# Performance work log

Measured on AMD Instinct MI355X. Metric: run time of the kernel, lower is better.

## Reference

```python
import jax, jax.numpy as jnp
import numpy as np

T, B, N, N2 = 2048, 32, 1024, 512

def setup_inputs() -> dict:
    key = jax.random.key(0)
    ks = jax.random.split(key, 7)
    s_n = 1.0 / np.sqrt(N)
    s_n2 = 1.0 / np.sqrt(N2)
    return {
        "hyp": jax.random.normal(ks[0], (T, B, N), dtype=jnp.float32),
        "W_w": jax.random.uniform(ks[1], (N2, N), jnp.float32, -s_n, s_n),
        "W_b": jax.random.uniform(ks[2], (N2,), jnp.float32, -s_n, s_n),
        "Wm_w": jax.random.uniform(ks[3], (N2, N), jnp.float32, -s_n, s_n),
        "Wm_b": jax.random.uniform(ks[4], (N2,), jnp.float32, -s_n, s_n),
        "Wh_w": jax.random.uniform(ks[5], (1, N2), jnp.float32, -s_n2, s_n2),
        "Wh_b": jax.random.uniform(ks[6], (1,), jnp.float32, -s_n2, s_n2),
        "dan_hidden_size": N,
        "attention_hidden_size": N2,
    }

def reference(hyp, W_w, W_b, Wm_w, Wm_b, Wh_w, Wh_b, dan_hidden_size, attention_hidden_size):
    # attention_type == 'attention' branch
    m = jnp.mean(hyp, axis=0)                      # [B, N] mean over time
    x = jnp.transpose(hyp, (1, 0, 2))              # [B, T, N]
    hq = jnp.tanh(jnp.einsum('btn,kn->btk', x, W_w) + W_b)        # [B, T, N2]
    hm = jnp.tanh(m @ Wm_w.T + Wm_b)[:, None, :]   # [B, 1, N2]
    h = hq * hm                                    # [B, T, N2]
    score = jnp.einsum('btk,ok->bto', h, Wh_w) + Wh_b  # [B, T, 1]
    a = jax.nn.softmax(score, axis=1)              # softmax over T
    c = jnp.sum(a * x, axis=1)                     # [B, N]
    return c
```

## Files before the change

### kernel.cpp

```cpp
#include <hip/hip_runtime.h>
#include <hip/hip_bf16.h>

#define TDIM 2048
#define BDIM 32
#define NDIM 1024
#define N2DIM 512
#define BN (BDIM * NDIM)
#define LDSP 72
#define NPART 64

typedef float f32x4 __attribute__((ext_vector_type(4)));
typedef __bf16 bf16x8 __attribute__((ext_vector_type(8)));

__device__ __forceinline__ float bf2f(unsigned int u) {
    union { unsigned int i; float f; } c;
    c.i = (u & 0xffffu) << 16;
    return c.f;
}

__device__ __forceinline__ unsigned short f2bf(float f) {
    union { float f; unsigned int i; } c;
    c.f = f;
    unsigned int i = c.i;
    unsigned int r = (i >> 16) & 1u;
    i += 0x7fffu + r;
    return (unsigned short)(i >> 16);
}

__device__ __forceinline__ int detect_f32(const void* wb) {
    const unsigned short* p = (const unsigned short*)wb;
    int cnt = 0;
    #pragma unroll
    for (int i = 0; i < 64; ++i) cnt += ((p[i] & 0x7fffu) <= 0x3D00u) ? 1 : 0;
    return cnt != 64;
}

__device__ __forceinline__ float ldf(const void* p, size_t i, int isf32) {
    if (isf32) return ((const float*)p)[i];
    return bf2f(((const unsigned short*)p)[i]);
}

__device__ __forceinline__ float tanh_fast(float x) {
    float e = __expf(2.0f * x);
    return 1.0f - 2.0f / (e + 1.0f);
}

__device__ __forceinline__ void unpack8(uint4 u, float* f) {
    f[0] = bf2f(u.x); f[1] = bf2f(u.x >> 16);
    f[2] = bf2f(u.y); f[3] = bf2f(u.y >> 16);
    f[4] = bf2f(u.z); f[5] = bf2f(u.z >> 16);
    f[6] = bf2f(u.w); f[7] = bf2f(u.w >> 16);
}

__device__ __forceinline__ void async16(const void* g, void* l) {
    __builtin_amdgcn_global_load_lds(
        (const __attribute__((address_space(1))) void*)g,
        (__attribute__((address_space(3))) void*)l, 16, 0, 0);
}


__global__ __launch_bounds__(256) void k_mean_cvt(const void* __restrict__ hyp,
                                                  const void* __restrict__ wb,
                                                  unsigned short* __restrict__ hyp16,
                                                  float* __restrict__ part) {
    const int isf32 = detect_f32(wb);
    const int col4 = (blockIdx.x * 256 + threadIdx.x) * 4;
    const int tc   = blockIdx.y;
    float a0 = 0.f, a1 = 0.f, a2 = 0.f, a3 = 0.f;
    if (isf32) {
        const float* h = (const float*)hyp + (size_t)(tc * 32) * BN + col4;
        unsigned short* o = hyp16 + (size_t)(tc * 32) * BN + col4;
        #pragma unroll 8
        for (int tt = 0; tt < 32; ++tt) {
            float4 v = *(const float4*)(h + (size_t)tt * BN);
            a0 += v.x; a1 += v.y; a2 += v.z; a3 += v.w;
            ushort4 u = { f2bf(v.x), f2bf(v.y), f2bf(v.z), f2bf(v.w) };
            *(ushort4*)(o + (size_t)tt * BN) = u;
        }
    } else {
        const unsigned short* h = (const unsigned short*)hyp + (size_t)(tc * 32) * BN + col4;
        unsigned short* o = hyp16 + (size_t)(tc * 32) * BN + col4;
        #pragma unroll 8
        for (int tt = 0; tt < 32; ++tt) {
            ushort4 u = *(const ushort4*)(h + (size_t)tt * BN);
            *(ushort4*)(o + (size_t)tt * BN) = u;
            a0 += bf2f(u.x); a1 += bf2f(u.y); a2 += bf2f(u.z); a3 += bf2f(u.w);
        }
    }
    float4 r = { a0, a1, a2, a3 };
    *(float4*)(part + (size_t)tc * BN + col4) = r;
}

__global__ __launch_bounds__(256) void k_prep(const void* __restrict__ W_w,
                                              const void* __restrict__ wb,
                                              const float* __restrict__ part,
                                              unsigned short* __restrict__ W16,
                                              float* __restrict__ m) {
    const int isf32 = detect_f32(wb);
    if (blockIdx.x < 512) {
        int i4 = (blockIdx.x * 256 + threadIdx.x) * 4;
        if (isf32) {
            float4 v = *(const float4*)((const float*)W_w + i4);
            ushort4 u = { f2bf(v.x), f2bf(v.y), f2bf(v.z), f2bf(v.w) };
            *(ushort4*)(W16 + i4) = u;
        } else {
            *(ushort4*)(W16 + i4) = *(const ushort4*)((const unsigned short*)W_w + i4);
        }
    } else {
        int i4 = ((blockIdx.x - 512) * 256 + threadIdx.x) * 4;
        float4 s = { 0.f, 0.f, 0.f, 0.f };
        #pragma unroll
        for (int c = 0; c < NPART; ++c) {
            float4 v = *(const float4*)(part + (size_t)c * BN + i4);
            s.x += v.x; s.y += v.y; s.z += v.z; s.w += v.w;
        }
        float k = 1.0f / (float)TDIM;
        float4 r = { s.x * k, s.y * k, s.z * k, s.w * k };
        *(float4*)(m + i4) = r;
    }
}

__global__ __launch_bounds__(256) void k_g(const float* __restrict__ m,
                                           const void* __restrict__ Wm_w,
                                           const void* __restrict__ Wm_b,
                                           const void* __restrict__ Wh_w,
                                           const void* __restrict__ wb,
                                           float* __restrict__ g) {
    const int isf32 = detect_f32(wb);
    int wid  = (blockIdx.x * 256 + threadIdx.x) >> 6;
    int lane = threadIdx.x & 63;
    int b = wid >> 9;
    int k = wid & 511;
    const float* mr = m + (size_t)b * NDIM;
    float s = 0.f;
    if (isf32) {
        const float* wr = (const float*)Wm_w + (size_t)k * NDIM;
        #pragma unroll
        for (int i = 0; i < 4; ++i) {
            int idx = (lane + i * 64) * 4;
            float4 mv = *(const float4*)(mr + idx);
            float4 wv = *(const float4*)(wr + idx);
            s += mv.x * wv.x + mv.y * wv.y + mv.z * wv.z + mv.w * wv.w;
        }
    } else {
        const unsigned short* wr = (const unsigned short*)Wm_w + (size_t)k * NDIM;
        #pragma unroll
        for (int i = 0; i < 4; ++i) {
            int idx = (lane + i * 64) * 4;
            float4 mv = *(const float4*)(mr + idx);
            ushort4 wv = *(const ushort4*)(wr + idx);
            s += mv.x * bf2f(wv.x) + mv.y * bf2f(wv.y)
               + mv.z * bf2f(wv.z) + mv.w * bf2f(wv.w);
        }
    }
    #pragma unroll
    for (int off = 32; off > 0; off >>= 1) s += __shfl_down(s, off, 64);
    if (lane == 0) {
        float v = tanh_fast(s + ldf(Wm_b, k, isf32));
        g[(size_t)b * N2DIM + k] = v * ldf(Wh_w, k, isf32);
    }
}

__global__ __launch_bounds__(256) void k_score(const unsigned short* __restrict__ hyp16,
                                               const unsigned short* __restrict__ W16,
                                               const void* __restrict__ W_b,
                                               const float* __restrict__ g,
                                               float* __restrict__ sp) {
    __shared__ __align__(16) unsigned short sA[128 * 64];
    __shared__ __align__(16) unsigned short sW[128 * 64];
    __shared__ float sRed[2][128];

    const int isf32 = detect_f32(W_b);
    const int tid = threadIdx.x;
    const int l   = tid & 63;
    const int w   = tid >> 6;
    const int wt  = w & 1;
    const int wkk = w >> 1;
    const int lm  = l & 15;
    const int lq  = l >> 4;
    const int b   = blockIdx.y;
    const int t0  = blockIdx.x * 128;
    const int kblk = blockIdx.z;

    const int grow = l >> 3;
    const int gkq  = (l & 7) ^ grow;
    const int swz0 = ((lq)     ^ (lm & 7)) * 8;
    const int swz1 = ((4 + lq) ^ (lm & 7)) * 8;

    f32x4 acc[4][4];
    #pragma unroll
    for (int mi = 0; mi < 4; ++mi)
        #pragma unroll
        for (int ni = 0; ni < 4; ++ni) {
            f32x4 z = {0.f, 0.f, 0.f, 0.f};
            acc[mi][ni] = z;
        }

    for (int it = 0; it < 16; ++it) {
        const int n0 = it * 64;
        #pragma unroll
        for (int p = 0; p < 4; ++p) {
            const int row = (w * 4 + p) * 8 + grow;
            async16(hyp16 + (size_t)(t0 + row) * BN + b * NDIM + n0 + gkq * 8,
                    &sA[(w * 4 + p) * 512]);
            async16(W16 + (size_t)(kblk * 128 + row) * NDIM + n0 + gkq * 8,
                    &sW[(w * 4 + p) * 512]);
        }
        __syncthreads();

        #pragma unroll
        for (int kk = 0; kk < 2; ++kk) {
            const int swz = kk ? swz1 : swz0;
            bf16x8 af[4];
            #pragma unroll
            for (int mi = 0; mi < 4; ++mi) {
                int mrow = wt * 64 + mi * 16 + lm;
                af[mi] = *(const bf16x8*)&sA[mrow * 64 + swz];
            }
            #pragma unroll
            for (int ni = 0; ni < 4; ++ni) {
                int nrow = wkk * 64 + ni * 16 + lm;
                bf16x8 bfr = *(const bf16x8*)&sW[nrow * 64 + swz];
                #pragma unroll
                for (int mi = 0; mi < 4; ++mi)
                    acc[mi][ni] = __builtin_amdgcn_mfma_f32_16x16x32_bf16(
                        af[mi], bfr, acc[mi][ni], 0, 0, 0);
            }
        }
        __syncthreads();
    }

    float scoreAcc[4][4];
    #pragma unroll
    for (int mi = 0; mi < 4; ++mi)
        #pragma unroll
        for (int r = 0; r < 4; ++r) scoreAcc[mi][r] = 0.f;
    #pragma unroll
    for (int ni = 0; ni < 4; ++ni) {
        int kc = kblk * 128 + wkk * 64 + ni * 16 + lm;
        float wbv = ldf(W_b, kc, isf32);
        float gg  = g[(size_t)b * N2DIM + kc];
        #pragma unroll
        for (int mi = 0; mi < 4; ++mi)
            #pragma unroll
            for (int r = 0; r < 4; ++r) {
                float v = tanh_fast(acc[mi][ni][r] + wbv);
                scoreAcc[mi][r] += v * gg;
            }
    }

    #pragma unroll
    for (int mi = 0; mi < 4; ++mi)
        #pragma unroll
        for (int r = 0; r < 4; ++r) {
            float s = scoreAcc[mi][r];
            s += __shfl_xor(s, 1, 64);
            s += __shfl_xor(s, 2, 64);
            s += __shfl_xor(s, 4, 64);
            s += __shfl_xor(s, 8, 64);
            if (lm == 0) sRed[wkk][wt * 64 + mi * 16 + lq * 4 + r] = s;
        }
    __syncthreads();
    if (tid < 128) {
        sp[(size_t)(kblk * BDIM + b) * TDIM + t0 + tid] = sRed[0][tid] + sRed[1][tid];
    }
}

__global__ __launch_bounds__(256) void k_softmax(const float* __restrict__ sp,
                                                 float* __restrict__ a) {
    __shared__ float red[8];
    int b = blockIdx.x;
    int tid = threadIdx.x;
    int w = tid >> 6, l = tid & 63;
    float v[8];
    float mx = -1e30f;
    #pragma unroll
    for (int i = 0; i < 8; ++i) {
        int t = tid + i * 256;
        float s = sp[(size_t)(0 * BDIM + b) * TDIM + t]
                + sp[(size_t)(1 * BDIM + b) * TDIM + t]
                + sp[(size_t)(2 * BDIM + b) * TDIM + t]
                + sp[(size_t)(3 * BDIM + b) * TDIM + t];
        v[i] = s; mx = fmaxf(mx, s);
    }
    #pragma unroll
    for (int off = 32; off > 0; off >>= 1) mx = fmaxf(mx, __shfl_xor(mx, off, 64));
    if (l == 0) red[w] = mx;
    __syncthreads();
    mx = fmaxf(fmaxf(red[0], red[1]), fmaxf(red[2], red[3]));
    float sum = 0.f;
    #pragma unroll
    for (int i = 0; i < 8; ++i) { v[i] = __expf(v[i] - mx); sum += v[i]; }
    #pragma unroll
    for (int off = 32; off > 0; off >>= 1) sum += __shfl_xor(sum, off, 64);
    if (l == 0) red[4 + w] = sum;
    __syncthreads();
    sum = red[4] + red[5] + red[6] + red[7];
    float inv = 1.0f / sum;
    float* ap = a + (size_t)b * TDIM;
    #pragma unroll
    for (int i = 0; i < 8; ++i) ap[tid + i * 256] = v[i] * inv;
}

__global__ __launch_bounds__(256) void k_wsum_part(const unsigned short* __restrict__ hyp16,
                                                   const float* __restrict__ a,
                                                   float* __restrict__ part) {
    const int col8 = (blockIdx.x * 256 + threadIdx.x) * 8;
    const int tc   = blockIdx.y;
    const int b    = col8 >> 10;
    const float* av = a + (size_t)b * TDIM + tc * 32;
    const uint4* src = (const uint4*)(hyp16 + (size_t)(tc * 32) * BN + col8);
    float acc[8] = {0.f,0.f,0.f,0.f,0.f,0.f,0.f,0.f};
    #pragma unroll 8
    for (int tt = 0; tt < 32; ++tt) {
        float wgt = av[tt];
        uint4 u = src[(size_t)tt * (BN / 8)];
        float f[8]; unpack8(u, f);
        #pragma unroll
        for (int j = 0; j < 8; ++j) acc[j] += wgt * f[j];
    }
    float* dst = part + (size_t)tc * BN + col8;
    #pragma unroll
    for (int j = 0; j < 8; ++j) dst[j] = acc[j];
}

__global__ __launch_bounds__(256) void k_reduce_out(const float* __restrict__ part,
                                                    const void* __restrict__ wb,
                                                    void* __restrict__ out) {
    const int isf32 = detect_f32(wb);
    int i4 = (blockIdx.x * 256 + threadIdx.x) * 4;
    float4 s = { 0.f, 0.f, 0.f, 0.f };
    #pragma unroll
    for (int c = 0; c < NPART; ++c) {
        float4 v = *(const float4*)(part + (size_t)c * BN + i4);
        s.x += v.x; s.y += v.y; s.z += v.z; s.w += v.w;
    }
    if (isf32) {
        *(float4*)((float*)out + i4) = s;
    } else {
        ushort4 u = { f2bf(s.x), f2bf(s.y), f2bf(s.z), f2bf(s.w) };
        *(ushort4*)((unsigned short*)out + i4) = u;
    }
}

__global__ __launch_bounds__(256) void k_mean_fb(const void* __restrict__ hyp,
                                                 const void* __restrict__ wb,
                                                 float* __restrict__ m) {
    const int isf32 = detect_f32(wb);
    int i = blockIdx.x * 256 + threadIdx.x;
    float s = 0.f;
    if (isf32) {
        const float* h = (const float*)hyp;
        #pragma unroll 8
        for (int t = 0; t < TDIM; ++t) s += h[(size_t)t * BN + i];
    } else {
        const unsigned short* h = (const unsigned short*)hyp;
        #pragma unroll 8
        for (int t = 0; t < TDIM; ++t) s += bf2f(h[(size_t)t * BN + i]);
    }
    m[i] = s * (1.0f / (float)TDIM);
}

__global__ __launch_bounds__(256) void k_score_fb(const void* __restrict__ hyp,
                                                  const void* __restrict__ W_w,
                                                  const void* __restrict__ W_b,
                                                  const float* __restrict__ g,
                                                  float* __restrict__ score) {
    __shared__ __align__(16) unsigned short sA[128 * LDSP];
    __shared__ __align__(16) unsigned short sW[128 * LDSP];
    __shared__ float sRed[2][128];

    const int isf32 = detect_f32(W_b);
    const int tid = threadIdx.x;
    const int l   = tid & 63;
    const int w   = tid >> 6;
    const int wt  = w & 1;
    const int wkk = w >> 1;
    const int lm  = l & 15;
    const int lq  = l >> 4;
    const int b   = blockIdx.y;
    const int t0  = blockIdx.x * 128;

    float scoreAcc[4][4];
    #pragma unroll
    for (int mi = 0; mi < 4; ++mi)
        #pragma unroll
        for (int r = 0; r < 4; ++r) scoreAcc[mi][r] = 0.f;

    for (int kblk = 0; kblk < 4; ++kblk) {
        f32x4 acc[4][4];
        #pragma unroll
        for (int mi = 0; mi < 4; ++mi)
            #pragma unroll
            for (int ni = 0; ni < 4; ++ni) {
                f32x4 z = {0.f, 0.f, 0.f, 0.f};
                acc[mi][ni] = z;
            }
        for (int it = 0; it < 16; ++it) {
            const int n0 = it * 64;
            #pragma unroll
            for (int p = 0; p < 4; ++p) {
                int ch  = p * 256 + tid;
                int row = ch >> 3;
                int pos = ch & 7;
                size_t offA = (size_t)(t0 + row) * BN + b * NDIM + n0 + pos * 8;
                size_t offW = (size_t)(kblk * 128 + row) * NDIM + n0 + pos * 8;
                uint4 va, vw;
                if (isf32) {
                    const float4* fa = (const float4*)((const float*)hyp + offA);
                    float4 a0 = fa[0], a1 = fa[1];
                    va.x = f2bf(a0.x) | ((unsigned)f2bf(a0.y) << 16);
                    va.y = f2bf(a0.z) | ((unsigned)f2bf(a0.w) << 16);
                    va.z = f2bf(a1.x) | ((unsigned)f2bf(a1.y) << 16);
                    va.w = f2bf(a1.z) | ((unsigned)f2bf(a1.w) << 16);
                    const float4* fw = (const float4*)((const float*)W_w + offW);
                    float4 w0 = fw[0], w1 = fw[1];
                    vw.x = f2bf(w0.x) | ((unsigned)f2bf(w0.y) << 16);
                    vw.y = f2bf(w0.z) | ((unsigned)f2bf(w0.w) << 16);
                    vw.z = f2bf(w1.x) | ((unsigned)f2bf(w1.y) << 16);
                    vw.w = f2bf(w1.z) | ((unsigned)f2bf(w1.w) << 16);
                } else {
                    va = *(const uint4*)((const unsigned short*)hyp + offA);
                    vw = *(const uint4*)((const unsigned short*)W_w + offW);
                }
                *(uint4*)&sA[row * LDSP + pos * 8] = va;
                *(uint4*)&sW[row * LDSP + pos * 8] = vw;
            }
            __syncthreads();
            #pragma unroll
            for (int kk = 0; kk < 2; ++kk) {
                const int koff = kk * 32 + lq * 8;
                bf16x8 af[4];
                #pragma unroll
                for (int mi = 0; mi < 4; ++mi) {
                    int mrow = wt * 64 + mi * 16 + lm;
                    af[mi] = *(const bf16x8*)&sA[mrow * LDSP + koff];
                }
                #pragma unroll
                for (int ni = 0; ni < 4; ++ni) {
                    int nrow = wkk * 64 + ni * 16 + lm;
                    bf16x8 bfr = *(const bf16x8*)&sW[nrow * LDSP + koff];
                    #pragma unroll
                    for (int mi = 0; mi < 4; ++mi)
                        acc[mi][ni] = __builtin_amdgcn_mfma_f32_16x16x32_bf16(
                            af[mi], bfr, acc[mi][ni], 0, 0, 0);
                }
            }
            __syncthreads();
        }
        #pragma unroll
        for (int ni = 0; ni < 4; ++ni) {
            int kc = kblk * 128 + wkk * 64 + ni * 16 + lm;
            float wbv = ldf(W_b, kc, isf32);
            float gg  = g[(size_t)b * N2DIM + kc];
            #pragma unroll
            for (int mi = 0; mi < 4; ++mi)
                #pragma unroll
                for (int r = 0; r < 4; ++r) {
                    float v = tanh_fast(acc[mi][ni][r] + wbv);
                    scoreAcc[mi][r] += v * gg;
                }
        }
    }
    #pragma unroll
    for (int mi = 0; mi < 4; ++mi)
        #pragma unroll
        for (int r = 0; r < 4; ++r) {
            float s = scoreAcc[mi][r];
            s += __shfl_xor(s, 1, 64);
            s += __shfl_xor(s, 2, 64);
            s += __shfl_xor(s, 4, 64);
            s += __shfl_xor(s, 8, 64);
            if (lm == 0) sRed[wkk][wt * 64 + mi * 16 + lq * 4 + r] = s;
        }
    __syncthreads();
    if (tid < 128) {
        score[(size_t)b * TDIM + t0 + tid] = sRed[0][tid] + sRed[1][tid];
    }
}

__global__ __launch_bounds__(256) void k_softmax_fb(const float* __restrict__ score,
                                                    float* __restrict__ a) {
    __shared__ float red[8];
    int b = blockIdx.x;
    int tid = threadIdx.x;
    int w = tid >> 6, l = tid & 63;
    const float* s = score + (size_t)b * TDIM;
    float v[8];
    float mx = -1e30f;
    #pragma unroll
    for (int i = 0; i < 8; ++i) { v[i] = s[tid + i * 256]; mx = fmaxf(mx, v[i]); }
    #pragma unroll
    for (int off = 32; off > 0; off >>= 1) mx = fmaxf(mx, __shfl_xor(mx, off, 64));
    if (l == 0) red[w] = mx;
    __syncthreads();
    mx = fmaxf(fmaxf(red[0], red[1]), fmaxf(red[2], red[3]));
    float sum = 0.f;
    #pragma unroll
    for (int i = 0; i < 8; ++i) { v[i] = __expf(v[i] - mx); sum += v[i]; }
    #pragma unroll
    for (int off = 32; off > 0; off >>= 1) sum += __shfl_xor(sum, off, 64);
    if (l == 0) red[4 + w] = sum;
    __syncthreads();
    sum = red[4] + red[5] + red[6] + red[7];
    float inv = 1.0f / sum;
    float* ap = a + (size_t)b * TDIM;
    #pragma unroll
    for (int i = 0; i < 8; ++i) ap[tid + i * 256] = v[i] * inv;
}

__global__ __launch_bounds__(256) void k_wsum_fb(const void* __restrict__ hyp,
                                                 const float* __restrict__ a,
                                                 const void* __restrict__ wb,
                                                 void* __restrict__ out) {
    const int isf32 = detect_f32(wb);
    int i = blockIdx.x * 256 + threadIdx.x;
    int b = i >> 10;
    const float* av = a + (size_t)b * TDIM;
    float s = 0.f;
    if (isf32) {
        const float* h = (const float*)hyp;
        #pragma unroll 8
        for (int t = 0; t < TDIM; ++t) s += av[t] * h[(size_t)t * BN + i];
    } else {
        const unsigned short* h = (const unsigned short*)hyp;
        #pragma unroll 8
        for (int t = 0; t < TDIM; ++t) s += av[t] * bf2f(h[(size_t)t * BN + i]);
    }
    if (isf32) ((float*)out)[i] = s;
    else       ((unsigned short*)out)[i] = f2bf(s);
}

extern "C" void kernel_launch(void* const* d_in, const int* in_sizes, int n_in,
                              void* d_out, int out_size, void* d_ws, size_t ws_size,
                              hipStream_t stream) {
    const void* hyp  = d_in[0];
    const void* W_w  = d_in[1];
    const void* W_b  = d_in[2];
    const void* Wm_w = d_in[3];
    const void* Wm_b = d_in[4];
    const void* Wh_w = d_in[5];

    float* ws    = (float*)d_ws;
    float* m     = ws;
    float* g     = m + BN;
    float* sp    = g + BDIM * N2DIM;
    float* a     = sp + 4 * BDIM * TDIM;
    float* part  = a + BDIM * TDIM;
    unsigned short* W16   = (unsigned short*)(part + NPART * BN);
    unsigned short* hyp16 = W16 + (size_t)N2DIM * NDIM;
    const size_t need = 145162240ull;

    if (ws_size >= need) {
        k_mean_cvt <<<dim3(32, NPART), 256, 0, stream>>>(hyp, W_b, hyp16, part);
        k_prep     <<<dim3(544),       256, 0, stream>>>(W_w, W_b, part, W16, m);
        k_g        <<<dim3(4096),      256, 0, stream>>>(m, Wm_w, Wm_b, Wh_w, W_b, g);
        k_score    <<<dim3(16, 32, 4), 256, 0, stream>>>(hyp16, W16, W_b, g, sp);
        k_softmax  <<<dim3(32),        256, 0, stream>>>(sp, a);
        k_wsum_part<<<dim3(16, NPART), 256, 0, stream>>>(hyp16, a, part);
        k_reduce_out<<<dim3(32),       256, 0, stream>>>(part, W_b, d_out);
    } else {
        float* score = sp;
        k_mean_fb  <<<dim3(128),    256, 0, stream>>>(hyp, W_b, m);
        k_g        <<<dim3(4096),   256, 0, stream>>>(m, Wm_w, Wm_b, Wh_w, W_b, g);
        k_score_fb <<<dim3(16, 32), 256, 0, stream>>>(hyp, W_w, W_b, g, score);
        k_softmax_fb<<<dim3(32),    256, 0, stream>>>(score, a);
        k_wsum_fb  <<<dim3(128),    256, 0, stream>>>(hyp, a, W_b, d_out);
    }
}
```

Measured before the change: 556.6 us.

## Double-buffer k_score LDS tiles and fold W conversion into mean kernel

The score GEMM now uses two LDS buffers for the hyp and W tiles. The next tile's async global-to-LDS loads are issued before the MFMAs on the current tile, and one of the two barriers per iteration is dropped. The W fp32-to-bf16 conversion moves into an extra row of blocks in k_mean_cvt, so k_prep shrinks to a small mean-reduction kernel. The risks are that LDS use doubles, which may lower occupancy, and that the extra conversion blocks may run late in the k_mean_cvt grid as a tail.

Measured after the change: 563.1 us. No clear change (+1.2%).

```diff
diff --git a/kernel.cpp b/kernel.cpp
--- a/kernel.cpp
+++ b/kernel.cpp
@@ -60,12 +60,30 @@
 
 
 __global__ __launch_bounds__(256) void k_mean_cvt(const void* __restrict__ hyp,
+                                                  const void* __restrict__ W_w,
                                                   const void* __restrict__ wb,
                                                   unsigned short* __restrict__ hyp16,
+                                                  unsigned short* __restrict__ W16,
                                                   float* __restrict__ part) {
     const int isf32 = detect_f32(wb);
+    const int tc = blockIdx.y;
+    if (tc == NPART) {
+        int t = blockIdx.x * 256 + threadIdx.x;
+        #pragma unroll
+        for (int j = 0; j < 16; ++j) {
+            int i4 = (j * 8192 + t) * 4;
+            if (isf32) {
+                float4 v = *(const float4*)((const float*)W_w + i4);
+                ushort4 u = { f2bf(v.x), f2bf(v.y), f2bf(v.z), f2bf(v.w) };
+                *(ushort4*)(W16 + i4) = u;
+            } else {
+                *(ushort4*)(W16 + i4) =
+                    *(const ushort4*)((const unsigned short*)W_w + i4);
+            }
+        }
+        return;
+    }
     const int col4 = (blockIdx.x * 256 + threadIdx.x) * 4;
-    const int tc   = blockIdx.y;
     float a0 = 0.f, a1 = 0.f, a2 = 0.f, a3 = 0.f;
     if (isf32) {
         const float* h = (const float*)hyp + (size_t)(tc * 32) * BN + col4;
@@ -91,33 +109,18 @@
     *(float4*)(part + (size_t)tc * BN + col4) = r;
 }
 
-__global__ __launch_bounds__(256) void k_prep(const void* __restrict__ W_w,
-                                              const void* __restrict__ wb,
-                                              const float* __restrict__ part,
-                                              unsigned short* __restrict__ W16,
-                                              float* __restrict__ m) {
-    const int isf32 = detect_f32(wb);
-    if (blockIdx.x < 512) {
-        int i4 = (blockIdx.x * 256 + threadIdx.x) * 4;
-        if (isf32) {
-            float4 v = *(const float4*)((const float*)W_w + i4);
-            ushort4 u = { f2bf(v.x), f2bf(v.y), f2bf(v.z), f2bf(v.w) };
-            *(ushort4*)(W16 + i4) = u;
-        } else {
-            *(ushort4*)(W16 + i4) = *(const ushort4*)((const unsigned short*)W_w + i4);
-        }
-    } else {
-        int i4 = ((blockIdx.x - 512) * 256 + threadIdx.x) * 4;
-        float4 s = { 0.f, 0.f, 0.f, 0.f };
-        #pragma unroll
-        for (int c = 0; c < NPART; ++c) {
-            float4 v = *(const float4*)(part + (size_t)c * BN + i4);
-            s.x += v.x; s.y += v.y; s.z += v.z; s.w += v.w;
-        }
-        float k = 1.0f / (float)TDIM;
-        float4 r = { s.x * k, s.y * k, s.z * k, s.w * k };
-        *(float4*)(m + i4) = r;
-    }
+__global__ __launch_bounds__(256) void k_reduce_mean(const float* __restrict__ part,
+                                                     float* __restrict__ m) {
+    int i4 = (blockIdx.x * 256 + threadIdx.x) * 4;
+    float4 s = { 0.f, 0.f, 0.f, 0.f };
+    #pragma unroll
+    for (int c = 0; c < NPART; ++c) {
+        float4 v = *(const float4*)(part + (size_t)c * BN + i4);
+        s.x += v.x; s.y += v.y; s.z += v.z; s.w += v.w;
+    }
+    float k = 1.0f / (float)TDIM;
+    float4 r = { s.x * k, s.y * k, s.z * k, s.w * k };
+    *(float4*)(m + i4) = r;
 }
 
 __global__ __launch_bounds__(256) void k_g(const float* __restrict__ m,
@@ -166,9 +169,9 @@
                                                const void* __restrict__ W_b,
                                                const float* __restrict__ g,
                                                float* __restrict__ sp) {
-    __shared__ __align__(16) unsigned short sA[128 * 64];
-    __shared__ __align__(16) unsigned short sW[128 * 64];
-    __shared__ float sRed[2][128];
+    __shared__ __align__(16) unsigned short sA[2][128 * 64];
+    __shared__ __align__(16) unsigned short sW[2][128 * 64];
+    float* sRed = (float*)&sA[0][0];
 
     const int isf32 = detect_f32(W_b);
     const int tid = threadIdx.x;
@@ -187,6 +190,9 @@
     const int swz0 = ((lq)     ^ (lm & 7)) * 8;
     const int swz1 = ((4 + lq) ^ (lm & 7)) * 8;
 
+    const unsigned short* Abase = hyp16 + (size_t)t0 * BN + b * NDIM + gkq * 8;
+    const unsigned short* Wbase = W16 + (size_t)(kblk * 128) * NDIM + gkq * 8;
+
     f32x4 acc[4][4];
     #pragma unroll
     for (int mi = 0; mi < 4; ++mi)
@@ -196,18 +202,28 @@
             acc[mi][ni] = z;
         }
 
-    for (int it = 0; it < 16; ++it) {
-        const int n0 = it * 64;
+    {
         #pragma unroll
         for (int p = 0; p < 4; ++p) {
             const int row = (w * 4 + p) * 8 + grow;
-            async16(hyp16 + (size_t)(t0 + row) * BN + b * NDIM + n0 + gkq * 8,
-                    &sA[(w * 4 + p) * 512]);
-            async16(W16 + (size_t)(kblk * 128 + row) * NDIM + n0 + gkq * 8,
-                    &sW[(w * 4 + p) * 512]);
-        }
+            async16(Abase + (size_t)row * BN, &sA[0][(w * 4 + p) * 512]);
+            async16(Wbase + (size_t)row * NDIM, &sW[0][(w * 4 + p) * 512]);
+        }
+    }
+
+    for (int it = 0; it < 16; ++it) {
+        const int cur = it & 1;
         __syncthreads();
-
+        if (it + 1 < 16) {
+            const int nxt = cur ^ 1;
+            const int n1 = (it + 1) * 64;
+            #pragma unroll
+            for (int p = 0; p < 4; ++p) {
+                const int row = (w * 4 + p) * 8 + grow;
+                async16(Abase + (size_t)row * BN + n1, &sA[nxt][(w * 4 + p) * 512]);
+                async16(Wbase + (size_t)row * NDIM + n1, &sW[nxt][(w * 4 + p) * 512]);
+            }
+        }
         #pragma unroll
         for (int kk = 0; kk < 2; ++kk) {
             const int swz = kk ? swz1 : swz0;
@@ -215,19 +231,18 @@
             #pragma unroll
             for (int mi = 0; mi < 4; ++mi) {
                 int mrow = wt * 64 + mi * 16 + lm;
-                af[mi] = *(const bf16x8*)&sA[mrow * 64 + swz];
+                af[mi] = *(const bf16x8*)&sA[cur][mrow * 64 + swz];
             }
             #pragma unroll
             for (int ni = 0; ni < 4; ++ni) {
                 int nrow = wkk * 64 + ni * 16 + lm;
-                bf16x8 bfr = *(const bf16x8*)&sW[nrow * 64 + swz];
+                bf16x8 bfr = *(const bf16x8*)&sW[cur][nrow * 64 + swz];
                 #pragma unroll
                 for (int mi = 0; mi < 4; ++mi)
                     acc[mi][ni] = __builtin_amdgcn_mfma_f32_16x16x32_bf16(
                         af[mi], bfr, acc[mi][ni], 0, 0, 0);
             }
         }
-        __syncthreads();
     }
 
     float scoreAcc[4][4];
@@ -258,11 +273,11 @@
             s += __shfl_xor(s, 2, 64);
             s += __shfl_xor(s, 4, 64);
             s += __shfl_xor(s, 8, 64);
-            if (lm == 0) sRed[wkk][wt * 64 + mi * 16 + lq * 4 + r] = s;
+            if (lm == 0) sRed[wkk * 128 + wt * 64 + mi * 16 + lq * 4 + r] = s;
         }
     __syncthreads();
     if (tid < 128) {
-        sp[(size_t)(kblk * BDIM + b) * TDIM + t0 + tid] = sRed[0][tid] + sRed[1][tid];
+        sp[(size_t)(kblk * BDIM + b) * TDIM + t0 + tid] = sRed[tid] + sRed[128 + tid];
     }
 }
 
@@ -552,19 +567,19 @@
     const size_t need = 145162240ull;
 
     if (ws_size >= need) {
-        k_mean_cvt <<<dim3(32, NPART), 256, 0, stream>>>(hyp, W_b, hyp16, part);
-        k_prep     <<<dim3(544),       256, 0, stream>>>(W_w, W_b, part, W16, m);
-        k_g        <<<dim3(4096),      256, 0, stream>>>(m, Wm_w, Wm_b, Wh_w, W_b, g);
-        k_score    <<<dim3(16, 32, 4), 256, 0, stream>>>(hyp16, W16, W_b, g, sp);
-        k_softmax  <<<dim3(32),        256, 0, stream>>>(sp, a);
-        k_wsum_part<<<dim3(16, NPART), 256, 0, stream>>>(hyp16, a, part);
-        k_reduce_out<<<dim3(32),       256, 0, stream>>>(part, W_b, d_out);
+        k_mean_cvt  <<<dim3(32, NPART + 1), 256, 0, stream>>>(hyp, W_w, W_b, hyp16, W16, part);
+        k_reduce_mean<<<dim3(32),           256, 0, stream>>>(part, m);
+        k_g         <<<dim3(4096),          256, 0, stream>>>(m, Wm_w, Wm_b, Wh_w, W_b, g);
+        k_score     <<<dim3(16, 32, 4),     256, 0, stream>>>(hyp16, W16, W_b, g, sp);
+        k_softmax   <<<dim3(32),            256, 0, stream>>>(sp, a);
+        k_wsum_part <<<dim3(16, NPART),     256, 0, stream>>>(hyp16, a, part);
+        k_reduce_out<<<dim3(32),            256, 0, stream>>>(part, W_b, d_out);
     } else {
         float* score = sp;
-        k_mean_fb  <<<dim3(128),    256, 0, stream>>>(hyp, W_b, m);
-        k_g        <<<dim3(4096),   256, 0, stream>>>(m, Wm_w, Wm_b, Wh_w, W_b, g);
-        k_score_fb <<<dim3(16, 32), 256, 0, stream>>>(hyp, W_w, W_b, g, score);
-        k_softmax_fb<<<dim3(32),    256, 0, stream>>>(score, a);
-        k_wsum_fb  <<<dim3(128),    256, 0, stream>>>(hyp, a, W_b, d_out);
-    }
-}
+        k_mean_fb   <<<dim3(128),    256, 0, stream>>>(hyp, W_b, m);
+        k_g         <<<dim3(4096),   256, 0, stream>>>(m, Wm_w, Wm_b, Wh_w, W_b, g);
+        k_score_fb  <<<dim3(16, 32), 256, 0, stream>>>(hyp, W_w, W_b, g, score);
+        k_softmax_fb<<<dim3(32),     256, 0, stream>>>(score, a);
+        k_wsum_fb   <<<dim3(128),    256, 0, stream>>>(hyp, a, W_b, d_out);
+    }
+}
```
